# Kernel tuning notes

Hardware: AMD Instinct MI355X
Metric: run time of the kernel (lower is better)

Reference implementation:

```python
import jax, jax.numpy as jnp
import numpy as np

B = 2
D = 256          # conv_dim / d_model
NH = 8           # attention heads
NL = 3           # feature levels: res5, res4, res3 (forward iterates reversed)
NP = 4           # sampling points per head per level
NLAYERS = 6
FF = 1024
SHAPES = [(24, 24), (48, 48), (96, 96)]   # (H, W) per level in encoder order
LEN = sum(h * w for h, w in SHAPES)       # 12096
HD = D // NH


def group_norm(x, s, b, groups=32, eps=1e-5):
    Bb, C, H, W = x.shape
    xr = x.reshape(Bb, groups, C // groups, H, W)
    m = xr.mean((2, 3, 4), keepdims=True)
    v = xr.var((2, 3, 4), keepdims=True)
    xr = (xr - m) * jax.lax.rsqrt(v + eps)
    return xr.reshape(Bb, C, H, W) * s[:, None, None] + b[:, None, None]


def layer_norm(x, s, b, eps=1e-5):
    m = x.mean(-1, keepdims=True)
    v = x.var(-1, keepdims=True)
    return (x - m) * jax.lax.rsqrt(v + eps) * s + b


def pos_embed_sine(H, W):
    # PositionEmbeddingSine(num_pos_feats=D//2, normalize=True), mask=None
    num = D // 2
    eps = 1e-6
    scale = 2.0 * np.pi
    y = (jnp.arange(1, H + 1, dtype=jnp.float32) / (H + eps)) * scale
    x = (jnp.arange(1, W + 1, dtype=jnp.float32) / (W + eps)) * scale
    dim_t = 10000.0 ** (2.0 * (jnp.arange(num) // 2).astype(jnp.float32) / num)
    def enc(v):
        p = v[:, None] / dim_t
        return jnp.stack([jnp.sin(p[:, 0::2]), jnp.cos(p[:, 1::2])], -1).reshape(v.shape[0], num)
    pe_y, pe_x = enc(y), enc(x)
    pos = jnp.concatenate([
        jnp.broadcast_to(pe_y[:, None, :], (H, W, num)),
        jnp.broadcast_to(pe_x[None, :, :], (H, W, num))], -1)
    return pos.transpose(2, 0, 1)  # [D, H, W]


def ms_deform_sample(value, loc, attn):
    # value [B,LEN,NH,HD]; loc [B,LEN,NH,NL,NP,2] in [0,1] (x,y); attn [B,LEN,NH,NL,NP]
    # Equivalent to grid_sample(bilinear, padding=zeros, align_corners=False) per level.
    out = jnp.zeros((B * NH, LEN, HD), jnp.float32)
    start = 0
    for lvl, (H, W) in enumerate(SHAPES):
        v = value[:, start:start + H * W].transpose(0, 2, 1, 3).reshape(B * NH, H * W, HD)
        l = loc[:, :, :, lvl].transpose(0, 2, 1, 3, 4).reshape(B * NH, LEN * NP, 2)
        x = l[..., 0] * W - 0.5
        y = l[..., 1] * H - 0.5
        x0f = jnp.floor(x); y0f = jnp.floor(y)
        wx = x - x0f; wy = y - y0f
        x0 = x0f.astype(jnp.int32); y0 = y0f.astype(jnp.int32)
        def gather(yi, xi):
            valid = (xi >= 0) & (xi < W) & (yi >= 0) & (yi < H)
            idx = jnp.clip(yi, 0, H - 1) * W + jnp.clip(xi, 0, W - 1)
            g = jnp.take_along_axis(v, idx[..., None], axis=1)
            return g * valid[..., None]
        s = (gather(y0, x0) * ((1 - wx) * (1 - wy))[..., None]
             + gather(y0, x0 + 1) * (wx * (1 - wy))[..., None]
             + gather(y0 + 1, x0) * ((1 - wx) * wy)[..., None]
             + gather(y0 + 1, x0 + 1) * (wx * wy)[..., None])
        w = attn[:, :, :, lvl].transpose(0, 2, 1, 3).reshape(B * NH, LEN * NP)
        out = out + (s * w[..., None]).reshape(B * NH, LEN, NP, HD).sum(2)
        start += H * W
    return out.reshape(B, NH, LEN, HD).transpose(0, 2, 1, 3).reshape(B, LEN, D)


def upsample_bilinear(x, Ho, Wo):
    # F.interpolate(mode='bilinear', align_corners=False)
    Bb, C, H, W = x.shape
    ys = jnp.maximum((jnp.arange(Ho, dtype=jnp.float32) + 0.5) * (H / Ho) - 0.5, 0.0)
    xs = jnp.maximum((jnp.arange(Wo, dtype=jnp.float32) + 0.5) * (W / Wo) - 0.5, 0.0)
    y0 = jnp.floor(ys).astype(jnp.int32); wy = ys - y0
    x0 = jnp.floor(xs).astype(jnp.int32); wx = xs - x0
    y1 = jnp.minimum(y0 + 1, H - 1); x1 = jnp.minimum(x0 + 1, W - 1)
    r = x[:, :, y0, :] * (1 - wy)[None, None, :, None] + x[:, :, y1, :] * wy[None, None, :, None]
    return r[:, :, :, x0] * (1 - wx)[None, None, None, :] + r[:, :, :, x1] * wx[None, None, None, :]


def conv1x1(x, w):
    return jnp.einsum('bchw,oc->bohw', x, w)


def _forward(res2, res3, res4, res5,
             pw5, pb5, gs5, gb5, pw4, pb4, gs4, gb4, pw3, pb3, gs3, gb3,
             level_embed, off_w, off_b, aw_w, aw_b, val_w, val_b, out_w, out_b,
             ln1_s, ln1_b, ffn1_w, ffn1_b, ffn2_w, ffn2_b, ln2_s, ln2_b,
             lat_w, lat_gs, lat_gb, fpn_w, fpn_gs, fpn_gb):
    feats = [res5, res4, res3]  # transformer_in_features reversed (coarse -> fine)
    projs = [(pw5, pb5, gs5, gb5), (pw4, pb4, gs4, gb4), (pw3, pb3, gs3, gb3)]
    src_list, pos_list = [], []
    for f, (pw, pb, gs, gb) in zip(feats, projs):
        s = group_norm(conv1x1(f, pw) + pb[:, None, None], gs, gb)
        src_list.append(s.reshape(B, D, -1).transpose(0, 2, 1))
        pos_list.append(pos_embed_sine(f.shape[2], f.shape[3]))
    src = jnp.concatenate(src_list, axis=1)  # [B, LEN, D]
    pos = jnp.concatenate([p.reshape(D, -1).T + level_embed[i]
                           for i, p in enumerate(pos_list)], axis=0)[None]  # [1, LEN, D]
    # reference points (x, y), valid_ratios == 1 (no padding masks)
    refs = []
    for H, W in SHAPES:
        gy, gx = jnp.meshgrid((jnp.arange(H, dtype=jnp.float32) + 0.5) / H,
                              (jnp.arange(W, dtype=jnp.float32) + 0.5) / W, indexing='ij')
        refs.append(jnp.stack([gx.ravel(), gy.ravel()], -1))
    ref_pts = jnp.broadcast_to(jnp.concatenate(refs, 0)[None, :, None, :], (B, LEN, NL, 2))
    norm_wh = jnp.array([[W, H] for H, W in SHAPES], jnp.float32)  # offset normalizer (x=W, y=H)
    for l in range(NLAYERS):
        q = src + pos
        value = (src @ val_w[l] + val_b[l]).reshape(B, LEN, NH, HD)
        off = (q @ off_w[l] + off_b[l]).reshape(B, LEN, NH, NL, NP, 2)
        aw = jax.nn.softmax((q @ aw_w[l] + aw_b[l]).reshape(B, LEN, NH, NL * NP), -1)
        aw = aw.reshape(B, LEN, NH, NL, NP)
        loc = ref_pts[:, :, None, :, None, :] + off / norm_wh[None, None, None, :, None, :]
        attn = ms_deform_sample(value, loc, aw) @ out_w[l] + out_b[l]
        src = layer_norm(src + attn, ln1_s[l], ln1_b[l])
        h = jax.nn.relu(src @ ffn1_w[l] + ffn1_b[l]) @ ffn2_w[l] + ffn2_b[l]
        src = layer_norm(src + h, ln2_s[l], ln2_b[l])
    outs, start = [], 0
    for H, W in SHAPES:
        outs.append(src[:, start:start + H * W].transpose(0, 2, 1).reshape(B, D, H, W))
        start += H * W
    # FPN: single lateral/output level (res2)
    lat = group_norm(conv1x1(res2, lat_w), lat_gs, lat_gb)
    y = lat + upsample_bilinear(outs[-1], lat.shape[2], lat.shape[3])
    y = jax.lax.conv_general_dilated(y, fpn_w, (1, 1), 'SAME',
                                     dimension_numbers=('NCHW', 'OIHW', 'NCHW'))
    y = jax.nn.relu(group_norm(y, fpn_gs, fpn_gb))
    # returns (out[-1], out[0], multi_scale_features...) = (fpn, y_res5, y_res5, y_res4, y_res3)
    return y, outs[0], outs[1], outs[2]


def setup_inputs():
    ks = jax.random.split(jax.random.key(0), 40)
    def rn(i, shape, s=0.02):
        return jax.random.normal(ks[i], shape, jnp.float32) * s
    inp = {}
    inp['res2'] = jax.random.normal(ks[0], (B, 256, 192, 192), jnp.float32)
    inp['res3'] = jax.random.normal(ks[1], (B, 512, 96, 96), jnp.float32)
    inp['res4'] = jax.random.normal(ks[2], (B, 1024, 48, 48), jnp.float32)
    inp['res5'] = jax.random.normal(ks[3], (B, 2048, 24, 24), jnp.float32)
    for name, cin, i in [('5', 2048, 4), ('4', 1024, 5), ('3', 512, 6)]:
        inp['pw' + name] = rn(i, (D, cin))
        inp['pb' + name] = jnp.zeros((D,), jnp.float32)
        inp['gs' + name] = jnp.ones((D,), jnp.float32)
        inp['gb' + name] = jnp.zeros((D,), jnp.float32)
    inp['level_embed'] = rn(7, (NL, D), 1.0)
    inp['off_w'] = rn(8, (NLAYERS, D, NH * NL * NP * 2))
    inp['off_b'] = rn(9, (NLAYERS, NH * NL * NP * 2), 0.5)
    inp['aw_w'] = rn(10, (NLAYERS, D, NH * NL * NP))
    inp['aw_b'] = jnp.zeros((NLAYERS, NH * NL * NP), jnp.float32)
    inp['val_w'] = rn(11, (NLAYERS, D, D))
    inp['val_b'] = jnp.zeros((NLAYERS, D), jnp.float32)
    inp['out_w'] = rn(12, (NLAYERS, D, D))
    inp['out_b'] = jnp.zeros((NLAYERS, D), jnp.float32)
    inp['ln1_s'] = jnp.ones((NLAYERS, D), jnp.float32)
    inp['ln1_b'] = jnp.zeros((NLAYERS, D), jnp.float32)
    inp['ffn1_w'] = rn(13, (NLAYERS, D, FF))
    inp['ffn1_b'] = jnp.zeros((NLAYERS, FF), jnp.float32)
    inp['ffn2_w'] = rn(14, (NLAYERS, FF, D))
    inp['ffn2_b'] = jnp.zeros((NLAYERS, D), jnp.float32)
    inp['ln2_s'] = jnp.ones((NLAYERS, D), jnp.float32)
    inp['ln2_b'] = jnp.zeros((NLAYERS, D), jnp.float32)
    inp['lat_w'] = rn(15, (D, 256))
    inp['lat_gs'] = jnp.ones((D,), jnp.float32)
    inp['lat_gb'] = jnp.zeros((D,), jnp.float32)
    inp['fpn_w'] = rn(16, (D, D, 3, 3))
    inp['fpn_gs'] = jnp.ones((D,), jnp.float32)
    inp['fpn_gb'] = jnp.zeros((D,), jnp.float32)
    return inp


def reference(res2, res3, res4, res5,
              pw5, pb5, gs5, gb5, pw4, pb4, gs4, gb4, pw3, pb3, gs3, gb3,
              level_embed, off_w, off_b, aw_w, aw_b, val_w, val_b, out_w, out_b,
              ln1_s, ln1_b, ffn1_w, ffn1_b, ffn2_w, ffn2_b, ln2_s, ln2_b,
              lat_w, lat_gs, lat_gb, fpn_w, fpn_gs, fpn_gb):
    return _forward(res2, res3, res4, res5,
                    pw5, pb5, gs5, gb5, pw4, pb4, gs4, gb4, pw3, pb3, gs3, gb3,
                    level_embed, off_w, off_b, aw_w, aw_b, val_w, val_b, out_w, out_b,
                    ln1_s, ln1_b, ffn1_w, ffn1_b, ffn2_w, ffn2_b, ln2_s, ln2_b,
                    lat_w, lat_gs, lat_gb, fpn_w, fpn_gs, fpn_gb)
```

## Files before the change

### kernel.cpp

```cpp
#include <hip/hip_runtime.h>
#include <math.h>

#define NLEN 12096
#define BB 2

typedef __bf16 bhalf;
typedef bhalf bh8 __attribute__((ext_vector_type(8)));
typedef bhalf bh4 __attribute__((ext_vector_type(4)));
typedef float f32x4 __attribute__((ext_vector_type(4)));

__device__ __forceinline__ int swz(int row) { return (row >> 1) & 3; }

__device__ __forceinline__ int xcd_swz(int id, int nwg) {
  int q = nwg >> 3, r = nwg & 7;
  int xcd = id & 7, pos = id >> 3;
  int base = (xcd < r) ? xcd * (q + 1) : r * (q + 1) + (xcd - r) * q;
  return base + pos;
}

#define GLOAD_LDS16(g, l) \
  __builtin_amdgcn_global_load_lds( \
      (const __attribute__((address_space(1))) unsigned int*)(g), \
      (__attribute__((address_space(3))) unsigned int*)(l), 16, 0, 0)

__global__ __launch_bounds__(256) void bgemm_kernel(
    const bhalf* __restrict__ A, const bhalf* __restrict__ Bt,
    const float* __restrict__ bias, void* __restrict__ Cout,
    int M, int N, int K, long long sA, long long sB, long long sC,
    int outBf16, int relu)
{
  const int gx = gridDim.x, gy = gridDim.y;
  const int nwg = gx * gy * gridDim.z;
  int flat = (blockIdx.z * gy + blockIdx.y) * gx + blockIdx.x;
  int logical = xcd_swz(flat, nwg);
  const int bz = logical / (gx * gy);
  int rem = logical - bz * gx * gy;
  const int by = rem / gx;
  const int bx = rem - by * gx;

  A += bz * sA; Bt += bz * sB;
  const int m0 = by * 128, n0 = bx * 128;
  __shared__ __align__(16) bhalf As[128 * 32];
  __shared__ __align__(16) bhalf Bs[128 * 32];
  const int t = threadIdx.x;
  const int lane = t & 63;
  const int w = t >> 6;
  const int wbase = t & 192;
  const int wm = (w >> 1) * 64, wn = (w & 1) * 64;
  const int fr = lane & 15, fg = lane >> 4;
  f32x4 acc[4][4] = {};
  for (int k0 = 0; k0 < K; k0 += 32) {
#pragma unroll
    for (int j = 0; j < 2; ++j) {
      int id = t + j * 256;
      int row = id >> 2, up = id & 3;
      int kcg = ((up ^ swz(row)) * 8);
      int m = m0 + row; m = (m < M) ? m : (M - 1);
      GLOAD_LDS16(A + (long long)m * K + k0 + kcg, As + (wbase + j * 256) * 8);
      int n = n0 + row; n = (n < N) ? n : (N - 1);
      GLOAD_LDS16(Bt + (long long)n * K + k0 + kcg, Bs + (wbase + j * 256) * 8);
    }
    __syncthreads();
    bh8 af[4], bf[4];
#pragma unroll
    for (int mi = 0; mi < 4; ++mi) {
      int r = wm + mi * 16 + fr;
      af[mi] = *(const bh8*)(As + r * 32 + ((fg ^ swz(r)) * 8));
    }
#pragma unroll
    for (int ni = 0; ni < 4; ++ni) {
      int r = wn + ni * 16 + fr;
      bf[ni] = *(const bh8*)(Bs + r * 32 + ((fg ^ swz(r)) * 8));
    }
#pragma unroll
    for (int mi = 0; mi < 4; ++mi)
#pragma unroll
      for (int ni = 0; ni < 4; ++ni)
        acc[mi][ni] = __builtin_amdgcn_mfma_f32_16x16x32_bf16(af[mi], bf[ni], acc[mi][ni], 0, 0, 0);
    __syncthreads();
  }
  float* Cf = (float*)Cout + bz * sC;
  bhalf* Cb = (bhalf*)Cout + bz * sC;
#pragma unroll
  for (int mi = 0; mi < 4; ++mi) {
#pragma unroll
    for (int r = 0; r < 4; ++r) {
      int m = m0 + wm + mi * 16 + fg * 4 + r;
      if (m >= M) continue;
#pragma unroll
      for (int ni = 0; ni < 4; ++ni) {
        int n = n0 + wn + ni * 16 + fr;
        if (n >= N) continue;
        float v = acc[mi][ni][r];
        if (bias) v += bias[n];
        if (relu) v = fmaxf(v, 0.f);
        if (outBf16) Cb[(long long)m * N + n] = (bhalf)v;
        else         Cf[(long long)m * N + n] = v;
      }
    }
  }
}

__global__ __launch_bounds__(256) void bgemm_ln_kernel(
    const bhalf* __restrict__ A, const bhalf* __restrict__ Bt,
    const float* __restrict__ bias,
    float* __restrict__ src, bhalf* __restrict__ srcb,
    bhalf* __restrict__ qbOut, const float* __restrict__ pos,
    const float* __restrict__ ls, const float* __restrict__ lb,
    int M, int K)
{
  const int nwg = gridDim.x;
  const int bid = xcd_swz(blockIdx.x, nwg);
  const int m0 = bid * 64;
  __shared__ __align__(16) bhalf Ls[320 * 32];
  bhalf* AsL = Ls;
  bhalf* BsL = Ls + 64 * 32;
  __shared__ float shS[64][2], shQ[64][2];
  const int t = threadIdx.x;
  const int lane = t & 63;
  const int w = t >> 6;
  const int wbase = t & 192;
  const int wm = (w >> 1) * 32, wn = (w & 1) * 128;
  const int fr = lane & 15, fg = lane >> 4;
  f32x4 acc[2][8] = {};
  for (int k0 = 0; k0 < K; k0 += 32) {
#pragma unroll
    for (int j = 0; j < 5; ++j) {
      int id = t + j * 256;
      int row = id >> 2, up = id & 3;
      int kcg = ((up ^ swz(row)) * 8);
      const bhalf* gsrc = (row < 64)
          ? (A + (long long)(m0 + row) * K + k0 + kcg)
          : (Bt + (long long)(row - 64) * K + k0 + kcg);
      GLOAD_LDS16(gsrc, Ls + (wbase + j * 256) * 8);
    }
    __syncthreads();
    bh8 af[2], bf[8];
#pragma unroll
    for (int mi = 0; mi < 2; ++mi) {
      int r = wm + mi * 16 + fr;
      af[mi] = *(const bh8*)(AsL + r * 32 + ((fg ^ swz(r)) * 8));
    }
#pragma unroll
    for (int ni = 0; ni < 8; ++ni) {
      int r = wn + ni * 16 + fr;
      bf[ni] = *(const bh8*)(BsL + r * 32 + ((fg ^ swz(r)) * 8));
    }
#pragma unroll
    for (int mi = 0; mi < 2; ++mi)
#pragma unroll
      for (int ni = 0; ni < 8; ++ni)
        acc[mi][ni] = __builtin_amdgcn_mfma_f32_16x16x32_bf16(af[mi], bf[ni], acc[mi][ni], 0, 0, 0);
    __syncthreads();
  }
#pragma unroll
  for (int mi = 0; mi < 2; ++mi) {
#pragma unroll
    for (int r = 0; r < 4; ++r) {
      int rt = wm + mi * 16 + fg * 4 + r;
      long long gm = m0 + rt;
      float s = 0.f, q = 0.f;
#pragma unroll
      for (int ni = 0; ni < 8; ++ni) {
        int col = wn + ni * 16 + fr;
        float v = acc[mi][ni][r] + bias[col] + src[gm * 256 + col];
        acc[mi][ni][r] = v;
        s += v; q = fmaf(v, v, q);
      }
#pragma unroll
      for (int o = 1; o < 16; o <<= 1) { s += __shfl_xor(s, o); q += __shfl_xor(q, o); }
      if (fr == 0) { shS[rt][w & 1] = s; shQ[rt][w & 1] = q; }
    }
  }
  __syncthreads();
#pragma unroll
  for (int mi = 0; mi < 2; ++mi) {
#pragma unroll
    for (int r = 0; r < 4; ++r) {
      int rt = wm + mi * 16 + fg * 4 + r;
      long long gm = m0 + rt;
      float S = shS[rt][0] + shS[rt][1];
      float Q = shQ[rt][0] + shQ[rt][1];
      float mean = S * (1.f / 256.f);
      float var = Q * (1.f / 256.f) - mean * mean;
      float rstd = rsqrtf(var + 1e-5f);
      int prow = (int)(gm % NLEN);
#pragma unroll
      for (int ni = 0; ni < 8; ++ni) {
        int col = wn + ni * 16 + fr;
        float y = (acc[mi][ni][r] - mean) * rstd * ls[col] + lb[col];
        src[gm * 256 + col] = y;
        srcb[gm * 256 + col] = (bhalf)y;
        if (qbOut) qbOut[gm * 256 + col] = (bhalf)(y + pos[(long long)prow * 256 + col]);
      }
    }
  }
}

__global__ __launch_bounds__(256) void bgemm_conv_kernel(
    const bhalf* __restrict__ Ab, const bhalf* __restrict__ Bt,
    bhalf* __restrict__ Cout)
{
  const int gx = gridDim.x, gy = gridDim.y;
  const int nwg = gx * gy * gridDim.z;
  int flat = (blockIdx.z * gy + blockIdx.y) * gx + blockIdx.x;
  int logical = xcd_swz(flat, nwg);
  const int bz = logical / (gx * gy);
  int rem = logical - bz * gx * gy;
  const int by = rem / gx;
  const int bx = rem - by * gx;

  const bhalf* Apad = Ab + (long long)bz * 37636 * 256;
  const int m0 = by * 128, n0 = bx * 128;
  __shared__ __align__(16) bhalf As[128 * 32];
  __shared__ __align__(16) bhalf Bs[128 * 32];
  const int t = threadIdx.x;
  const int lane = t & 63;
  const int w = t >> 6;
  const int wbase = t & 192;
  const int wm = (w >> 1) * 64, wn = (w & 1) * 64;
  const int fr = lane & 15, fg = lane >> 4;
  int rowA[2], py[2], px[2], kcg[2];
#pragma unroll
  for (int j = 0; j < 2; ++j) {
    int id = t + j * 256;
    rowA[j] = id >> 2;
    kcg[j] = (((id & 3) ^ swz(rowA[j])) * 8);
    int m = m0 + rowA[j];
    py[j] = m / 192; px[j] = m % 192;
  }
  f32x4 acc[4][4] = {};
  for (int s = 0; s < 72; ++s) {
    const int cib = s / 9, tap = s % 9;
    const int ty = tap / 3, tx = tap % 3;
#pragma unroll
    for (int j = 0; j < 2; ++j) {
      GLOAD_LDS16(Apad + ((long long)(py[j] + ty) * 194 + px[j] + tx) * 256 + cib * 32 + kcg[j],
                  As + (wbase + j * 256) * 8);
      GLOAD_LDS16(Bt + (long long)(n0 + rowA[j]) * 2304 + s * 32 + kcg[j],
                  Bs + (wbase + j * 256) * 8);
    }
    __syncthreads();
    bh8 af[4], bf[4];
#pragma unroll
    for (int mi = 0; mi < 4; ++mi) {
      int r = wm + mi * 16 + fr;
      af[mi] = *(const bh8*)(As + r * 32 + ((fg ^ swz(r)) * 8));
    }
#pragma unroll
    for (int ni = 0; ni < 4; ++ni) {
      int r = wn + ni * 16 + fr;
      bf[ni] = *(const bh8*)(Bs + r * 32 + ((fg ^ swz(r)) * 8));
    }
#pragma unroll
    for (int mi = 0; mi < 4; ++mi)
#pragma unroll
      for (int ni = 0; ni < 4; ++ni)
        acc[mi][ni] = __builtin_amdgcn_mfma_f32_16x16x32_bf16(af[mi], bf[ni], acc[mi][ni], 0, 0, 0);
    __syncthreads();
  }
  bhalf* Cb = Cout + (long long)bz * 36864 * 256;
#pragma unroll
  for (int mi = 0; mi < 4; ++mi)
#pragma unroll
    for (int r = 0; r < 4; ++r) {
      int m = m0 + wm + mi * 16 + fg * 4 + r;
#pragma unroll
      for (int ni = 0; ni < 4; ++ni) {
        int n = n0 + wn + ni * 16 + fr;
        Cb[(long long)m * 256 + n] = (bhalf)acc[mi][ni][r];
      }
    }
}

__global__ void twcvt_kernel(const float* __restrict__ Wsrc, bhalf* __restrict__ out,
                             int Kd, int Nd, long long zdst)
{
  __shared__ float tile[32][33];
  long long zi = (long long)blockIdx.z * Kd * Nd;
  long long zo = (long long)blockIdx.z * zdst;
  int n0 = blockIdx.x * 32, k0 = blockIdx.y * 32;
#pragma unroll
  for (int j = 0; j < 4; ++j) {
    int kk = threadIdx.y + 8 * j;
    tile[kk][threadIdx.x] = Wsrc[zi + (long long)(k0 + kk) * Nd + n0 + threadIdx.x];
  }
  __syncthreads();
#pragma unroll
  for (int j = 0; j < 4; ++j) {
    int nn = threadIdx.y + 8 * j;
    out[zo + (long long)(n0 + nn) * Kd + k0 + threadIdx.x] = (bhalf)tile[threadIdx.x][nn];
  }
}

__global__ void tfeat_kernel(const float* __restrict__ Fsrc, bhalf* __restrict__ out,
                             int Ci, int HW)
{
  __shared__ float tile[32][33];
  long long zo = (long long)blockIdx.z * Ci * HW;
  int hw0 = blockIdx.x * 32, c0 = blockIdx.y * 32;
#pragma unroll
  for (int j = 0; j < 4; ++j) {
    int cc = threadIdx.y + 8 * j;
    tile[cc][threadIdx.x] = Fsrc[zo + (long long)(c0 + cc) * HW + hw0 + threadIdx.x];
  }
  __syncthreads();
#pragma unroll
  for (int j = 0; j < 4; ++j) {
    int hh = threadIdx.y + 8 * j;
    out[zo + (long long)(hw0 + hh) * Ci + c0 + threadIdx.x] = (bhalf)tile[threadIdx.x][hh];
  }
}

__global__ void cvt_kernel(const float* __restrict__ in, bhalf* __restrict__ out, int n)
{
  int i = blockIdx.x * 256 + threadIdx.x;
  if (i < n) out[i] = (bhalf)in[i];
}

__global__ void fpnw_kernel(const float* __restrict__ Wsrc, bhalf* __restrict__ out)
{
  int o = blockIdx.x * 256 + threadIdx.x;
  if (o >= 256 * 2304) return;
  int co = o / 2304, r = o % 2304;
  int cib = r / 288, rr = r % 288, tap = rr >> 5, cil = rr & 31;
  int ci = cib * 32 + cil;
  out[o] = (bhalf)Wsrc[(co * 256 + ci) * 9 + tap];
}

__global__ void biascat_kernel(const float* __restrict__ ob, const float* __restrict__ ab,
                               float* __restrict__ out)
{
  int l = blockIdx.x, t = threadIdx.x;
  if (t < 288) out[l * 288 + t] = (t < 192) ? ob[l * 192 + t] : ab[l * 96 + t - 192];
}

__global__ void border_zero_kernel(bhalf* __restrict__ latb)
{
  int idx = blockIdx.x * 256 + threadIdx.x;
  int total = BB * 4 * 194;
  if (idx >= total) return;
  int b = idx / (4 * 194);
  int r = idx - b * 4 * 194;
  int strip = r / 194, p = r % 194;
  int y, x;
  if (strip == 0)      { y = 0;   x = p; }
  else if (strip == 1) { y = 193; x = p; }
  else if (strip == 2) { y = p;   x = 0; }
  else                 { y = p;   x = 193; }
  uint4* dst = (uint4*)(latb + ((long long)b * 37636 + (long long)y * 194 + x) * 256);
#pragma unroll
  for (int j = 0; j < 32; ++j) dst[j] = make_uint4(0u, 0u, 0u, 0u);
}

__global__ void pos_kernel(float* __restrict__ pos, const float* __restrict__ level_embed)
{
  int i = blockIdx.x, c = threadIdx.x;
  int lvl, Wq, loc;
  if (i < 576)       { lvl = 0; Wq = 24; loc = i; }
  else if (i < 2880) { lvl = 1; Wq = 48; loc = i - 576; }
  else               { lvl = 2; Wq = 96; loc = i - 2880; }
  int h = loc / Wq, wcol = loc % Wq;
  int cc = c & 127;
  float coord = (c < 128) ? (float)(h + 1) : (float)(wcol + 1);
  float denom = (float)Wq + 1e-6f;
  float v = coord / denom * 6.28318530717958647692f;
  float tp = powf(10000.0f, (float)(cc & ~1) * (1.0f / 128.0f));
  float ang = v / tp;
  float val = (cc & 1) ? cosf(ang) : sinf(ang);
  pos[(long long)i * 256 + c] = val + level_embed[lvl * 256 + c];
}

__global__ __launch_bounds__(256) void gn_part_kernel(const void* __restrict__ X,
    float* __restrict__ part, int HW, int isBf16, int nch)
{
  const int b = blockIdx.y, ch = blockIdx.x;
  const int rows = (HW + nch - 1) / nch;
  const int r0 = ch * rows;
  const int r1 = min(r0 + rows, HW);
  const int cg = threadIdx.x & 31;
  const int ro = threadIdx.x >> 5;
  float s = 0.f, s2 = 0.f;
  if (isBf16) {
    const bhalf* p = (const bhalf*)X + (long long)b * HW * 256 + cg * 8;
    for (int r = r0 + ro; r < r1; r += 8) {
      bh8 v = *(const bh8*)(p + (long long)r * 256);
#pragma unroll
// ... 31 lines not shown
    long long o = ((long long)bg * nch + i) * 2;
    s += part[o]; s2 += part[o + 1];
  }
#pragma unroll
  for (int o = 32; o > 0; o >>= 1) { s += __shfl_down(s, o); s2 += __shfl_down(s2, o); }
  if (threadIdx.x == 0) {
    float inv = 1.f / (float)(HW * 8);
    float mean = s * inv;
    float var = s2 * inv - mean * mean;
    stats[bg * 2] = mean;
    stats[bg * 2 + 1] = rsqrtf(var + 1e-5f);
  }
}

__global__ void gn_apply_rm_kernel(const float* __restrict__ T, const float* __restrict__ stats,
    const float* __restrict__ gs, const float* __restrict__ gb,
    float* __restrict__ src, bhalf* __restrict__ srcb, bhalf* __restrict__ qb,
    const float* __restrict__ pos, int HW, int startRow)
{
  long long idx = (long long)blockIdx.x * 256 + threadIdx.x;
  int c = threadIdx.x & 255;
  long long row = idx >> 8;
  int b = (int)(row / HW);
  long long hw = row - (long long)b * HW;
  int g = c >> 3;
  float v = T[idx];
  v = (v - stats[(b * 32 + g) * 2]) * stats[(b * 32 + g) * 2 + 1] * gs[c] + gb[c];
  long long pr = (startRow + hw) * 256 + c;
  long long o = (long long)b * NLEN * 256 + pr;
  src[o] = v;
  srcb[o] = (bhalf)v;
  qb[o] = (bhalf)(v + pos[pr]);
}

__global__ __launch_bounds__(256) void deform_kernel(const bhalf* __restrict__ value,
    const bhalf* __restrict__ offaw, bhalf* __restrict__ out)
{
  const int t = threadIdx.x;
  const int q = t >> 5;
  const int sub = t & 31;
  const int bi = blockIdx.x * 8 + q;
  const int i = bi % NLEN;
  const int bbase = bi - i;
  const int c0 = sub * 8;
  const int head = sub >> 2;
  int loc, Wq;
  if (i < 576)       { Wq = 24; loc = i; }
  else if (i < 2880) { Wq = 48; loc = i - 576; }
  else               { Wq = 96; loc = i - 2880; }
  const float rx = ((loc % Wq) + 0.5f) / (float)Wq;
  const float ry = ((loc / Wq) + 0.5f) / (float)Wq;
  const bhalf* offp = offaw + (long long)bi * 288 + head * 24;
  const bhalf* awp  = offaw + (long long)bi * 288 + 192 + head * 12;
  float aw[12]; float mx = -1e30f;
#pragma unroll
  for (int j = 0; j < 12; ++j) { aw[j] = (float)awp[j]; mx = fmaxf(mx, aw[j]); }
  float ssum = 0.f;
#pragma unroll
  for (int j = 0; j < 12; ++j) { aw[j] = __expf(aw[j] - mx); ssum += aw[j]; }
  const float sinv = 1.f / ssum;
  float acc[8] = {};
  const int starts[3] = {0, 576, 2880};
  const int Ls[3] = {24, 48, 96};
#pragma unroll
  for (int l = 0; l < 3; ++l) {
    const int Wl = Ls[l];
    const float fW = (float)Wl;
    const bhalf* vb = value + (long long)(bbase + starts[l]) * 256 + c0;
#pragma unroll
    for (int p = 0; p < 4; ++p) {
      const float ox = (float)offp[l * 8 + p * 2], oy = (float)offp[l * 8 + p * 2 + 1];
      const float a = aw[l * 4 + p] * sinv;
      const float x = (rx + ox / fW) * fW - 0.5f;
      const float y = (ry + oy / fW) * fW - 0.5f;
      const float x0f = floorf(x), y0f = floorf(y);
      const float wx = x - x0f, wy = y - y0f;
      const int x0 = (int)x0f, y0 = (int)y0f;
      const int x1 = x0 + 1, y1 = y0 + 1;
      const bool xv0 = (x0 >= 0) & (x0 < Wl);
      const bool xv1 = (x1 >= 0) & (x1 < Wl);
      const bool yv0 = (y0 >= 0) & (y0 < Wl);
      const bool yv1 = (y1 >= 0) & (y1 < Wl);
      const int cx0 = min(max(x0, 0), Wl - 1), cx1 = min(max(x1, 0), Wl - 1);
      const int cy0 = min(max(y0, 0), Wl - 1), cy1 = min(max(y1, 0), Wl - 1);
      const float w00 = (xv0 && yv0) ? (1.f - wx) * (1.f - wy) * a : 0.f;
      const float w01 = (xv1 && yv0) ? wx * (1.f - wy) * a : 0.f;
      const float w10 = (xv0 && yv1) ? (1.f - wx) * wy * a : 0.f;
      const float w11 = (xv1 && yv1) ? wx * wy * a : 0.f;
      const bh8 g00 = *(const bh8*)(vb + (cy0 * Wl + cx0) * 256);
      const bh8 g01 = *(const bh8*)(vb + (cy0 * Wl + cx1) * 256);
      const bh8 g10 = *(const bh8*)(vb + (cy1 * Wl + cx0) * 256);
      const bh8 g11 = *(const bh8*)(vb + (cy1 * Wl + cx1) * 256);
#pragma unroll
      for (int e = 0; e < 8; ++e)
        acc[e] = fmaf(w00, (float)g00[e], fmaf(w01, (float)g01[e],
                 fmaf(w10, (float)g10[e], fmaf(w11, (float)g11[e], acc[e]))));
    }
  }
  bh8 o;
#pragma unroll
  for (int e = 0; e < 8; ++e) o[e] = (bhalf)acc[e];
  *(bh8*)(out + (long long)bi * 256 + c0) = o;
}

__global__ void transpose_out_kernel(const float* __restrict__ src, float* __restrict__ out,
    int HW, int startRow)
{
  __shared__ float tile[32][33];
  int b = blockIdx.z;
  int w0 = blockIdx.x * 32, c0 = blockIdx.y * 32;
#pragma unroll
  for (int j = 0; j < 4; ++j) {
    int wl = threadIdx.y + 8 * j;
    tile[wl][threadIdx.x] = src[((long long)b * NLEN + startRow + w0 + wl) * 256 + c0 + threadIdx.x];
  }
  __syncthreads();
#pragma unroll
  for (int j = 0; j < 4; ++j) {
    int cl = threadIdx.y + 8 * j;
    out[((long long)b * 256 + c0 + cl) * HW + w0 + threadIdx.x] = tile[threadIdx.x][cl];
  }
}

__global__ void lat_finish_rm_kernel(const bhalf* __restrict__ lat, const float* __restrict__ stats,
    const float* __restrict__ gs, const float* __restrict__ gb,
    const float* __restrict__ src, bhalf* __restrict__ latb)
{
  long long idx = (long long)blockIdx.x * 256 + threadIdx.x;
  int c = threadIdx.x & 255;
  long long row = idx >> 8;
  int b = (int)(row / 36864);
  int p = (int)(row - (long long)b * 36864);
  int y = p / 192, x = p % 192;
  int g = c >> 3;
  float v = (float)lat[idx];
  v = (v - stats[(b * 32 + g) * 2]) * stats[(b * 32 + g) * 2 + 1] * gs[c] + gb[c];
  float ys = fmaxf(y * 0.5f - 0.25f, 0.f);
  float xs = fmaxf(x * 0.5f - 0.25f, 0.f);
  int y0 = (int)ys; float wy = ys - (float)y0; int y1 = min(y0 + 1, 95);
  int x0 = (int)xs; float wx = xs - (float)x0; int x1 = min(x0 + 1, 95);
  const float* sp = src + ((long long)b * NLEN + 2880) * 256 + c;
  float r0 = sp[(long long)(y0 * 96 + x0) * 256] * (1.f - wx) + sp[(long long)(y0 * 96 + x1) * 256] * wx;
  float r1 = sp[(long long)(y1 * 96 + x0) * 256] * (1.f - wx) + sp[(long long)(y1 * 96 + x1) * 256] * wx;
  latb[((long long)b * 37636 + (long long)(y + 1) * 194 + (x + 1)) * 256 + c]
      = (bhalf)(v + r0 * (1.f - wy) + r1 * wy);
}

__global__ void gn_relu_tr_kernel(const bhalf* __restrict__ convC, const float* __restrict__ stats,
    const float* __restrict__ gs, const float* __restrict__ gb, float* __restrict__ Y)
{
  __shared__ float tile[32][33];
  int b = blockIdx.z;
  int hw0 = blockIdx.x * 32, c0 = blockIdx.y * 32;
#pragma unroll
  for (int j = 0; j < 4; ++j) {
    int hwl = threadIdx.y + 8 * j;
    int c = c0 + threadIdx.x;
    int g = c >> 3;
    float v = (float)convC[((long long)b * 36864 + hw0 + hwl) * 256 + c];
    v = (v - stats[(b * 32 + g) * 2]) * stats[(b * 32 + g) * 2 + 1] * gs[c] + gb[c];
    tile[hwl][threadIdx.x] = fmaxf(v, 0.f);
  }
  __syncthreads();
// ... 29 lines not shown
  const float* ln1_b = (const float*)d_in[26];
  const float* ffn1_w = (const float*)d_in[27];
  const float* ffn1_b = (const float*)d_in[28];
  const float* ffn2_w = (const float*)d_in[29];
  const float* ffn2_b = (const float*)d_in[30];
  const float* ln2_s = (const float*)d_in[31];
  const float* ln2_b = (const float*)d_in[32];
  const float* lat_w = (const float*)d_in[33];
  const float* lat_gs = (const float*)d_in[34];
  const float* lat_gb = (const float*)d_in[35];
  const float* fpn_w = (const float*)d_in[36];
  const float* fpn_gs = (const float*)d_in[37];
  const float* fpn_gb = (const float*)d_in[38];

  char* W = (char*)d_ws;
  float* src   = (float*)(W + 0);
  float* pos   = (float*)(W + 24772608LL);
  float* tmp   = (float*)(W + 37158912LL);
  bhalf* srcb  = (bhalf*)(W + 61931520LL);
  bhalf* wreg  = (bhalf*)(W + 74317824LL);
  float* stats = (float*)(W + 86212608LL);
  float* part  = (float*)(W + 86213120LL);
  float* offaw_b = (float*)(W + 86278656LL);
  char*  U     = W + 86286848LL;

  bhalf* valT   = wreg + 0;
  bhalf* offawT = wreg + 393216;
  bhalf* outT   = wreg + 835584;
  bhalf* f1T    = wreg + 1228800;
  bhalf* f2T    = wreg + 2801664;
  bhalf* pwb5   = wreg + 4374528;
  bhalf* pwb4   = wreg + 4898816;
  bhalf* pwb3   = wreg + 5160960;
  bhalf* latwb  = wreg + 5292032;
  bhalf* fpnT   = wreg + 5357568;

  bhalf* qb      = (bhalf*)(U + 0);
  bhalf* valueb  = (bhalf*)(U + 12386304LL);
  bhalf* sampb   = (bhalf*)(U + 24772608LL);
  bhalf* offbuf  = (bhalf*)(U + 37158912LL);
  bhalf* hbuf    = (bhalf*)(U + 65028096LL);
  bhalf* featT   = (bhalf*)(U + 24772608LL);
  bhalf* res2T   = (bhalf*)(U + 0);
  bhalf* latbf   = (bhalf*)(U + 37748736LL);
  bhalf* latb    = (bhalf*)(U + 75497472LL);

  float* Yout = (float*)d_out;
  float* out0 = Yout + 18874368LL;
  float* out1 = Yout + 19169280LL;
  float* out2 = Yout + 20348928LL;

  const int M = BB * NLEN;

  twcvt_kernel<<<dim3(8, 8, 6), dim3(32, 8), 0, stream>>>(val_w, valT, 256, 256, 65536LL);
  twcvt_kernel<<<dim3(6, 8, 6), dim3(32, 8), 0, stream>>>(off_w, offawT, 256, 192, 73728LL);
  twcvt_kernel<<<dim3(3, 8, 6), dim3(32, 8), 0, stream>>>(aw_w, offawT + 192 * 256, 256, 96, 73728LL);
  twcvt_kernel<<<dim3(8, 8, 6), dim3(32, 8), 0, stream>>>(out_w, outT, 256, 256, 65536LL);
  twcvt_kernel<<<dim3(32, 8, 6), dim3(32, 8), 0, stream>>>(ffn1_w, f1T, 256, 1024, 262144LL);
  twcvt_kernel<<<dim3(8, 32, 6), dim3(32, 8), 0, stream>>>(ffn2_w, f2T, 1024, 256, 262144LL);
  biascat_kernel<<<dim3(6), dim3(288), 0, stream>>>(off_b, aw_b, offaw_b);
  cvt_kernel<<<dim3(2048), dim3(256), 0, stream>>>(pw[0], pwb5, 524288);
  cvt_kernel<<<dim3(1024), dim3(256), 0, stream>>>(pw[1], pwb4, 262144);
  cvt_kernel<<<dim3(512),  dim3(256), 0, stream>>>(pw[2], pwb3, 131072);
  cvt_kernel<<<dim3(256),  dim3(256), 0, stream>>>(lat_w, latwb, 65536);
  fpnw_kernel<<<dim3(2304), dim3(256), 0, stream>>>(fpn_w, fpnT);

  pos_kernel<<<dim3(NLEN), dim3(256), 0, stream>>>(pos, level_embed);

  const float* feats[3] = {res5, res4, res3};
  const bhalf* pwbs[3] = {pwb5, pwb4, pwb3};
  const int cins[3] = {2048, 1024, 512};
  const int HWs[3] = {576, 2304, 9216};
  const int startsHost[3] = {0, 576, 2880};
  const int nchs[3] = {16, 64, 128};
  for (int lvl = 0; lvl < 3; ++lvl) {
    int HW = HWs[lvl], cin = cins[lvl], nch = nchs[lvl];
    tfeat_kernel<<<dim3(HW / 32, cin / 32, BB), dim3(32, 8), 0, stream>>>(feats[lvl], featT, cin, HW);
    bgemm_kernel<<<dim3(2, (HW + 127) / 128, BB), dim3(256), 0, stream>>>(
        featT, pwbs[lvl], pb[lvl], tmp, HW, 256, cin,
        (long long)HW * cin, 0LL, (long long)HW * 256, 0, 0);
    gn_part_kernel<<<dim3(nch, BB), dim3(256), 0, stream>>>(tmp, part, HW, 0, nch);
    gn_fin_kernel<<<dim3(64), dim3(64), 0, stream>>>(part, stats, nch, HW);
    gn_apply_rm_kernel<<<dim3(BB * HW), dim3(256), 0, stream>>>(
        tmp, stats, gss[lvl], gbb[lvl], src, srcb, qb, pos, HW, startsHost[lvl]);
  }

  for (int l = 0; l < 6; ++l) {
    bgemm_kernel<<<dim3(2, M / 128, 1), dim3(256), 0, stream>>>(
        srcb, valT + (long long)l * 65536, val_b + l * 256, valueb,
        M, 256, 256, 0LL, 0LL, 0LL, 1, 0);
    bgemm_kernel<<<dim3(3, M / 128, 1), dim3(256), 0, stream>>>(
        qb, offawT + (long long)l * 73728, offaw_b + l * 288, offbuf,
        M, 288, 256, 0LL, 0LL, 0LL, 1, 0);
    deform_kernel<<<dim3(M / 8), dim3(256), 0, stream>>>(valueb, offbuf, sampb);
    bgemm_ln_kernel<<<dim3(M / 64), dim3(256), 0, stream>>>(
        sampb, outT + (long long)l * 65536, out_b + l * 256,
        src, srcb, nullptr, pos, ln1_s + l * 256, ln1_b + l * 256, M, 256);
    bgemm_kernel<<<dim3(8, M / 128, 1), dim3(256), 0, stream>>>(
        srcb, f1T + (long long)l * 262144, ffn1_b + l * 1024, hbuf,
        M, 1024, 256, 0LL, 0LL, 0LL, 1, 1);
    bgemm_ln_kernel<<<dim3(M / 64), dim3(256), 0, stream>>>(
        hbuf, f2T + (long long)l * 262144, ffn2_b + l * 256,
        src, srcb, qb, pos, ln2_s + l * 256, ln2_b + l * 256, M, 1024);
  }

  float* outsPtr[3] = {out0, out1, out2};
  for (int lvl = 0; lvl < 3; ++lvl) {
    transpose_out_kernel<<<dim3(HWs[lvl] / 32, 8, BB), dim3(32, 8), 0, stream>>>(
        src, outsPtr[lvl], HWs[lvl], startsHost[lvl]);
  }

  tfeat_kernel<<<dim3(1152, 8, BB), dim3(32, 8), 0, stream>>>(res2, res2T, 256, 36864);
  bgemm_kernel<<<dim3(2, 288, BB), dim3(256), 0, stream>>>(
      res2T, latwb, nullptr, latbf, 36864, 256, 256,
      36864LL * 256, 0LL, 36864LL * 256, 1, 0);
  gn_part_kernel<<<dim3(128, BB), dim3(256), 0, stream>>>(latbf, part, 36864, 1, 128);
  gn_fin_kernel<<<dim3(64), dim3(64), 0, stream>>>(part, stats, 128, 36864);
  border_zero_kernel<<<dim3((BB * 4 * 194 + 255) / 256), dim3(256), 0, stream>>>(latb);
  lat_finish_rm_kernel<<<dim3(73728), dim3(256), 0, stream>>>(latbf, stats, lat_gs, lat_gb, src, latb);
  bgemm_conv_kernel<<<dim3(2, 288, BB), dim3(256), 0, stream>>>(latb, fpnT, latbf);
  gn_part_kernel<<<dim3(128, BB), dim3(256), 0, stream>>>(latbf, part, 36864, 1, 128);
  gn_fin_kernel<<<dim3(64), dim3(64), 0, stream>>>(part, stats, 128, 36864);
  gn_relu_tr_kernel<<<dim3(1152, 8, BB), dim3(32, 8), 0, stream>>>(latbf, stats, fpn_gs, fpn_gb, Yout);
}
```

Baseline: 1.771 ms.

## Narrow GEMM tiles, halve LN-GEMM row tile, merge prep and transpose launches

Measured after the change: 1.582 ms. 10.7% less time.

```diff
diff --git a/kernel.cpp b/kernel.cpp
--- a/kernel.cpp
+++ b/kernel.cpp
@@ -23,12 +23,18 @@
       (const __attribute__((address_space(1))) unsigned int*)(g), \
       (__attribute__((address_space(3))) unsigned int*)(l), 16, 0, 0)
 
-__global__ __launch_bounds__(256) void bgemm_kernel(
+template<int BNF>
+__global__ __launch_bounds__(256) void bgemm_t_kernel(
     const bhalf* __restrict__ A, const bhalf* __restrict__ Bt,
     const float* __restrict__ bias, void* __restrict__ Cout,
     int M, int N, int K, long long sA, long long sB, long long sC,
     int outBf16, int relu)
 {
+  constexpr int BN = BNF * 16;
+  constexpr int ROWS = 128 + BN;
+  constexpr int UNITS = ROWS * 4;
+  constexpr int ITERS = (UNITS + 255) / 256;
+  constexpr int NFR = BNF / 2;
   const int gx = gridDim.x, gy = gridDim.y;
   const int nwg = gx * gy * gridDim.z;
   int flat = (blockIdx.z * gy + blockIdx.y) * gx + blockIdx.x;
@@ -39,43 +45,49 @@
   const int bx = rem - by * gx;
 
   A += bz * sA; Bt += bz * sB;
-  const int m0 = by * 128, n0 = bx * 128;
-  __shared__ __align__(16) bhalf As[128 * 32];
-  __shared__ __align__(16) bhalf Bs[128 * 32];
+  const int m0 = by * 128, n0 = bx * BN;
+  __shared__ __align__(16) bhalf Ls[ROWS * 32];
   const int t = threadIdx.x;
   const int lane = t & 63;
   const int w = t >> 6;
   const int wbase = t & 192;
-  const int wm = (w >> 1) * 64, wn = (w & 1) * 64;
+  const int wm = (w >> 1) * 64, wn = (w & 1) * (BN / 2);
   const int fr = lane & 15, fg = lane >> 4;
-  f32x4 acc[4][4] = {};
+  f32x4 acc[4][NFR] = {};
   for (int k0 = 0; k0 < K; k0 += 32) {
 #pragma unroll
-    for (int j = 0; j < 2; ++j) {
-      int id = t + j * 256;
-      int row = id >> 2, up = id & 3;
-      int kcg = ((up ^ swz(row)) * 8);
-      int m = m0 + row; m = (m < M) ? m : (M - 1);
-      GLOAD_LDS16(A + (long long)m * K + k0 + kcg, As + (wbase + j * 256) * 8);
-      int n = n0 + row; n = (n < N) ? n : (N - 1);
-      GLOAD_LDS16(Bt + (long long)n * K + k0 + kcg, Bs + (wbase + j * 256) * 8);
+    for (int j = 0; j < ITERS; ++j) {
+      int u = t + j * 256;
+      if (UNITS % 256 == 0 || u < UNITS) {
+        int row = u >> 2, up = u & 3;
+        int kcg = ((up ^ swz(row)) * 8);
+        const bhalf* gsrc;
+        if (row < 128) {
+          int m = m0 + row; m = (m < M) ? m : (M - 1);
+          gsrc = A + (long long)m * K + k0 + kcg;
+        } else {
+          int n = n0 + row - 128; n = (n < N) ? n : (N - 1);
+          gsrc = Bt + (long long)n * K + k0 + kcg;
+        }
+        GLOAD_LDS16(gsrc, Ls + (long long)(wbase + j * 256) * 8);
+      }
     }
     __syncthreads();
-    bh8 af[4], bf[4];
+    bh8 af[4], bf[NFR];
 #pragma unroll
     for (int mi = 0; mi < 4; ++mi) {
       int r = wm + mi * 16 + fr;
-      af[mi] = *(const bh8*)(As + r * 32 + ((fg ^ swz(r)) * 8));
-    }
-#pragma unroll
-    for (int ni = 0; ni < 4; ++ni) {
-      int r = wn + ni * 16 + fr;
-      bf[ni] = *(const bh8*)(Bs + r * 32 + ((fg ^ swz(r)) * 8));
+      af[mi] = *(const bh8*)(Ls + r * 32 + ((fg ^ swz(r)) * 8));
+    }
+#pragma unroll
+    for (int ni = 0; ni < NFR; ++ni) {
+      int r = 128 + wn + ni * 16 + fr;
+      bf[ni] = *(const bh8*)(Ls + r * 32 + ((fg ^ swz(r)) * 8));
     }
 #pragma unroll
     for (int mi = 0; mi < 4; ++mi)
 #pragma unroll
-      for (int ni = 0; ni < 4; ++ni)
+      for (int ni = 0; ni < NFR; ++ni)
         acc[mi][ni] = __builtin_amdgcn_mfma_f32_16x16x32_bf16(af[mi], bf[ni], acc[mi][ni], 0, 0, 0);
     __syncthreads();
   }
@@ -88,7 +100,7 @@
       int m = m0 + wm + mi * 16 + fg * 4 + r;
       if (m >= M) continue;
 #pragma unroll
-      for (int ni = 0; ni < 4; ++ni) {
+      for (int ni = 0; ni < NFR; ++ni) {
         int n = n0 + wn + ni * 16 + fr;
         if (n >= N) continue;
         float v = acc[mi][ni][r];
@@ -111,88 +123,79 @@
 {
   const int nwg = gridDim.x;
   const int bid = xcd_swz(blockIdx.x, nwg);
-  const int m0 = bid * 64;
-  __shared__ __align__(16) bhalf Ls[320 * 32];
-  bhalf* AsL = Ls;
-  bhalf* BsL = Ls + 64 * 32;
-  __shared__ float shS[64][2], shQ[64][2];
+  const int m0 = bid * 32;
+  __shared__ __align__(16) bhalf Ls[288 * 32];
+  __shared__ float shS[32][2], shQ[32][2];
   const int t = threadIdx.x;
   const int lane = t & 63;
   const int w = t >> 6;
   const int wbase = t & 192;
-  const int wm = (w >> 1) * 32, wn = (w & 1) * 128;
+  const int wm = (w >> 1) * 16, wn = (w & 1) * 128;
   const int fr = lane & 15, fg = lane >> 4;
-  f32x4 acc[2][8] = {};
+  f32x4 acc[8] = {};
   for (int k0 = 0; k0 < K; k0 += 32) {
 #pragma unroll
     for (int j = 0; j < 5; ++j) {
-      int id = t + j * 256;
-      int row = id >> 2, up = id & 3;
-      int kcg = ((up ^ swz(row)) * 8);
-      const bhalf* gsrc = (row < 64)
-          ? (A + (long long)(m0 + row) * K + k0 + kcg)
-          : (Bt + (long long)(row - 64) * K + k0 + kcg);
-      GLOAD_LDS16(gsrc, Ls + (wbase + j * 256) * 8);
+      int u = t + j * 256;
+      if (u < 1152) {
+        int row = u >> 2, up = u & 3;
+        int kcg = ((up ^ swz(row)) * 8);
+        const bhalf* gsrc = (row < 32)
+            ? (A + (long long)(m0 + row) * K + k0 + kcg)
+            : (Bt + (long long)(row - 32) * K + k0 + kcg);
+        GLOAD_LDS16(gsrc, Ls + (long long)(wbase + j * 256) * 8);
+      }
     }
     __syncthreads();
-    bh8 af[2], bf[8];
-#pragma unroll
-    for (int mi = 0; mi < 2; ++mi) {
-      int r = wm + mi * 16 + fr;
-      af[mi] = *(const bh8*)(AsL + r * 32 + ((fg ^ swz(r)) * 8));
+    bh8 af, bf[8];
+    {
+      int r = wm + fr;
+      af = *(const bh8*)(Ls + r * 32 + ((fg ^ swz(r)) * 8));
     }
 #pragma unroll
     for (int ni = 0; ni < 8; ++ni) {
-      int r = wn + ni * 16 + fr;
-      bf[ni] = *(const bh8*)(BsL + r * 32 + ((fg ^ swz(r)) * 8));
-    }
-#pragma unroll
-    for (int mi = 0; mi < 2; ++mi)
-#pragma unroll
-      for (int ni = 0; ni < 8; ++ni)
-        acc[mi][ni] = __builtin_amdgcn_mfma_f32_16x16x32_bf16(af[mi], bf[ni], acc[mi][ni], 0, 0, 0);
+      int r = 32 + wn + ni * 16 + fr;
+      bf[ni] = *(const bh8*)(Ls + r * 32 + ((fg ^ swz(r)) * 8));
+    }
+#pragma unroll
+    for (int ni = 0; ni < 8; ++ni)
+      acc[ni] = __builtin_amdgcn_mfma_f32_16x16x32_bf16(af, bf[ni], acc[ni], 0, 0, 0);
     __syncthreads();
   }
 #pragma unroll
-  for (int mi = 0; mi < 2; ++mi) {
-#pragma unroll
-    for (int r = 0; r < 4; ++r) {
-      int rt = wm + mi * 16 + fg * 4 + r;
-      long long gm = m0 + rt;
-      float s = 0.f, q = 0.f;
-#pragma unroll
-      for (int ni = 0; ni < 8; ++ni) {
-        int col = wn + ni * 16 + fr;
-        float v = acc[mi][ni][r] + bias[col] + src[gm * 256 + col];
-        acc[mi][ni][r] = v;
-        s += v; q = fmaf(v, v, q);
-      }
-#pragma unroll
-      for (int o = 1; o < 16; o <<= 1) { s += __shfl_xor(s, o); q += __shfl_xor(q, o); }
-      if (fr == 0) { shS[rt][w & 1] = s; shQ[rt][w & 1] = q; }
-    }
+  for (int r = 0; r < 4; ++r) {
+    int rt = wm + fg * 4 + r;
+    long long gm = m0 + rt;
+    float s = 0.f, q = 0.f;
+#pragma unroll
+    for (int ni = 0; ni < 8; ++ni) {
+      int col = wn + ni * 16 + fr;
+      float v = acc[ni][r] + bias[col] + src[gm * 256 + col];
+      acc[ni][r] = v;
+      s += v; q = fmaf(v, v, q);
+    }
+#pragma unroll
+    for (int o = 1; o < 16; o <<= 1) { s += __shfl_xor(s, o); q += __shfl_xor(q, o); }
+    if (fr == 0) { shS[rt][w & 1] = s; shQ[rt][w & 1] = q; }
   }
   __syncthreads();
 #pragma unroll
-  for (int mi = 0; mi < 2; ++mi) {
-#pragma unroll
-    for (int r = 0; r < 4; ++r) {
-      int rt = wm + mi * 16 + fg * 4 + r;
-      long long gm = m0 + rt;
-      float S = shS[rt][0] + shS[rt][1];
-      float Q = shQ[rt][0] + shQ[rt][1];
-      float mean = S * (1.f / 256.f);
-      float var = Q * (1.f / 256.f) - mean * mean;
-      float rstd = rsqrtf(var + 1e-5f);
-      int prow = (int)(gm % NLEN);
-#pragma unroll
-      for (int ni = 0; ni < 8; ++ni) {
-        int col = wn + ni * 16 + fr;
-        float y = (acc[mi][ni][r] - mean) * rstd * ls[col] + lb[col];
-        src[gm * 256 + col] = y;
-        srcb[gm * 256 + col] = (bhalf)y;
-        if (qbOut) qbOut[gm * 256 + col] = (bhalf)(y + pos[(long long)prow * 256 + col]);
-      }
+  for (int r = 0; r < 4; ++r) {
+    int rt = wm + fg * 4 + r;
+    long long gm = m0 + rt;
+    float S = shS[rt][0] + shS[rt][1];
+    float Q = shQ[rt][0] + shQ[rt][1];
+    float mean = S * (1.f / 256.f);
+    float var = Q * (1.f / 256.f) - mean * mean;
+    float rstd = rsqrtf(var + 1e-5f);
+    int prow = (int)(gm % NLEN);
+#pragma unroll
+    for (int ni = 0; ni < 8; ++ni) {
+      int col = wn + ni * 16 + fr;
+      float y = (acc[ni][r] - mean) * rstd * ls[col] + lb[col];
+      src[gm * 256 + col] = y;
+      srcb[gm * 256 + col] = (bhalf)y;
+      if (qbOut) qbOut[gm * 256 + col] = (bhalf)(y + pos[(long long)prow * 256 + col]);
     }
   }
 }
@@ -273,13 +276,36 @@
     }
 }
 
-__global__ void twcvt_kernel(const float* __restrict__ Wsrc, bhalf* __restrict__ out,
-                             int Kd, int Nd, long long zdst)
-{
+__global__ void wprep_t_kernel(
+    const float* __restrict__ s0, const float* __restrict__ s1,
+    const float* __restrict__ s2, const float* __restrict__ s3,
+    const float* __restrict__ s4, const float* __restrict__ s5,
+    bhalf* __restrict__ d0, bhalf* __restrict__ d1, bhalf* __restrict__ d2,
+    bhalf* __restrict__ d3, bhalf* __restrict__ d4, bhalf* __restrict__ d5)
+{
+  const int KdA[6]  = {256, 256, 256, 256, 256, 1024};
+  const int NdA[6]  = {256, 192, 96, 256, 1024, 256};
+  const long long zdA[6] = {65536, 73728, 73728, 65536, 262144, 262144};
+  const int cum[6]  = {384, 672, 816, 1200, 2736, 4272};
+  int blk = blockIdx.x;
+  int seg = 0;
+#pragma unroll
+  for (int i = 0; i < 6; ++i) if (blk >= cum[i]) seg = i + 1;
+  int base = (seg == 0) ? 0 : cum[seg - 1];
+  int idx = blk - base;
+  const float* Wsrc = (seg == 0) ? s0 : (seg == 1) ? s1 : (seg == 2) ? s2
+                    : (seg == 3) ? s3 : (seg == 4) ? s4 : s5;
+  bhalf* out = (seg == 0) ? d0 : (seg == 1) ? d1 : (seg == 2) ? d2
+             : (seg == 3) ? d3 : (seg == 4) ? d4 : d5;
+  int Kd = KdA[seg], Nd = NdA[seg];
+  int nx = Nd / 32, ny = Kd / 32;
+  int z = idx / (nx * ny);
+  int r = idx - z * nx * ny;
+  int ky = r / nx, nxi = r - ky * nx;
   __shared__ float tile[32][33];
-  long long zi = (long long)blockIdx.z * Kd * Nd;
-  long long zo = (long long)blockIdx.z * zdst;
-  int n0 = blockIdx.x * 32, k0 = blockIdx.y * 32;
+  long long zi = (long long)z * Kd * Nd;
+  long long zo = (long long)z * zdA[seg];
+  int n0 = nxi * 32, k0 = ky * 32;
 #pragma unroll
   for (int j = 0; j < 4; ++j) {
     int kk = threadIdx.y + 8 * j;
@@ -293,6 +319,39 @@
   }
 }
 
+__global__ void wprep_m_kernel(
+    const float* __restrict__ fpn_w, bhalf* __restrict__ fpnT,
+    const float* __restrict__ pw5, bhalf* __restrict__ pwb5,
+    const float* __restrict__ pw4, bhalf* __restrict__ pwb4,
+    const float* __restrict__ pw3, bhalf* __restrict__ pwb3,
+    const float* __restrict__ lat_w, bhalf* __restrict__ latwb,
+    const float* __restrict__ ob, const float* __restrict__ ab,
+    float* __restrict__ offaw_b)
+{
+  int blk = blockIdx.x, t = threadIdx.x;
+  if (blk < 2304) {
+    int o = blk * 256 + t;
+    int co = o / 2304, r = o % 2304;
+    int cib = r / 288, rr = r % 288, tap = rr >> 5, cil = rr & 31;
+    int ci = cib * 32 + cil;
+    fpnT[o] = (bhalf)fpn_w[(co * 256 + ci) * 9 + tap];
+  } else if (blk < 4352) {
+    int i = (blk - 2304) * 256 + t; pwb5[i] = (bhalf)pw5[i];
+  } else if (blk < 5376) {
+    int i = (blk - 4352) * 256 + t; pwb4[i] = (bhalf)pw4[i];
+  } else if (blk < 5888) {
+    int i = (blk - 5376) * 256 + t; pwb3[i] = (bhalf)pw3[i];
+  } else if (blk < 6144) {
+    int i = (blk - 5888) * 256 + t; latwb[i] = (bhalf)lat_w[i];
+  } else {
+    int i = (blk - 6144) * 256 + t;
+    if (i < 6 * 288) {
+      int l = i / 288, c = i % 288;
+      offaw_b[i] = (c < 192) ? ob[l * 192 + c] : ab[l * 96 + c - 192];
+    }
+  }
+}
+
 __global__ void tfeat_kernel(const float* __restrict__ Fsrc, bhalf* __restrict__ out,
                              int Ci, int HW)
 {
@@ -310,29 +369,6 @@
     int hh = threadIdx.y + 8 * j;
     out[zo + (long long)(hw0 + hh) * Ci + c0 + threadIdx.x] = (bhalf)tile[threadIdx.x][hh];
   }
-}
-
-__global__ void cvt_kernel(const float* __restrict__ in, bhalf* __restrict__ out, int n)
-{
-  int i = blockIdx.x * 256 + threadIdx.x;
-  if (i < n) out[i] = (bhalf)in[i];
-}
-
-__global__ void fpnw_kernel(const float* __restrict__ Wsrc, bhalf* __restrict__ out)
-{
-  int o = blockIdx.x * 256 + threadIdx.x;
-  if (o >= 256 * 2304) return;
-  int co = o / 2304, r = o % 2304;
-  int cib = r / 288, rr = r % 288, tap = rr >> 5, cil = rr & 31;
-  int ci = cib * 32 + cil;
-  out[o] = (bhalf)Wsrc[(co * 256 + ci) * 9 + tap];
-}
-
-__global__ void biascat_kernel(const float* __restrict__ ob, const float* __restrict__ ab,
-                               float* __restrict__ out)
-{
-  int l = blockIdx.x, t = threadIdx.x;
-  if (t < 288) out[l * 288 + t] = (t < 192) ? ob[l * 192 + t] : ab[l * 96 + t - 192];
 }
 
 __global__ void border_zero_kernel(bhalf* __restrict__ latb)
@@ -470,12 +506,10 @@
   const float ry = ((loc / Wq) + 0.5f) / (float)Wq;
   const bhalf* offp = offaw + (long long)bi * 288 + head * 24;
   const bhalf* awp  = offaw + (long long)bi * 288 + 192 + head * 12;
-  float aw[12]; float mx = -1e30f;
-#pragma unroll
-  for (int j = 0; j < 12; ++j) { aw[j] = (float)awp[j]; mx = fmaxf(mx, aw[j]); }
+  float aw[12];
   float ssum = 0.f;
 #pragma unroll
-  for (int j = 0; j < 12; ++j) { aw[j] = __expf(aw[j] - mx); ssum += aw[j]; }
+  for (int j = 0; j < 12; ++j) { aw[j] = __expf((float)awp[j]); ssum += aw[j]; }
   const float sinv = 1.f / ssum;
   float acc[8] = {};
   const int starts[3] = {0, 576, 2880};
@@ -521,12 +555,20 @@
   *(bh8*)(out + (long long)bi * 256 + c0) = o;
 }
 
-__global__ void transpose_out_kernel(const float* __restrict__ src, float* __restrict__ out,
-    int HW, int startRow)
-{
+__global__ void transpose_out_kernel(const float* __restrict__ src,
+    float* __restrict__ out0, float* __restrict__ out1, float* __restrict__ out2)
+{
+  int blk = blockIdx.x;
+  int lvl, HW, startRow;
+  float* out;
+  if (blk < 288)       { lvl = 0; HW = 576;  startRow = 0;    out = out0; }
+  else if (blk < 1440) { lvl = 1; HW = 2304; startRow = 576;  out = out1; blk -= 288; }
+  else                 { lvl = 2; HW = 9216; startRow = 2880; out = out2; blk -= 1440; }
+  int nx = HW / 32;
+  int bx = blk % nx; int r = blk / nx;
+  int cy = r % 8; int b = r / 8;
   __shared__ float tile[32][33];
-  int b = blockIdx.z;
-  int w0 = blockIdx.x * 32, c0 = blockIdx.y * 32;
+  int w0 = bx * 32, c0 = cy * 32;
 #pragma unroll
   for (int j = 0; j < 4; ++j) {
     int wl = threadIdx.y + 8 * j;
@@ -662,18 +704,12 @@
 
   const int M = BB * NLEN;
 
-  twcvt_kernel<<<dim3(8, 8, 6), dim3(32, 8), 0, stream>>>(val_w, valT, 256, 256, 65536LL);
-  twcvt_kernel<<<dim3(6, 8, 6), dim3(32, 8), 0, stream>>>(off_w, offawT, 256, 192, 73728LL);
-  twcvt_kernel<<<dim3(3, 8, 6), dim3(32, 8), 0, stream>>>(aw_w, offawT + 192 * 256, 256, 96, 73728LL);
-  twcvt_kernel<<<dim3(8, 8, 6), dim3(32, 8), 0, stream>>>(out_w, outT, 256, 256, 65536LL);
-  twcvt_kernel<<<dim3(32, 8, 6), dim3(32, 8), 0, stream>>>(ffn1_w, f1T, 256, 1024, 262144LL);
-  twcvt_kernel<<<dim3(8, 32, 6), dim3(32, 8), 0, stream>>>(ffn2_w, f2T, 1024, 256, 262144LL);
-  biascat_kernel<<<dim3(6), dim3(288), 0, stream>>>(off_b, aw_b, offaw_b);
-  cvt_kernel<<<dim3(2048), dim3(256), 0, stream>>>(pw[0], pwb5, 524288);
-  cvt_kernel<<<dim3(1024), dim3(256), 0, stream>>>(pw[1], pwb4, 262144);
-  cvt_kernel<<<dim3(512),  dim3(256), 0, stream>>>(pw[2], pwb3, 131072);
-  cvt_kernel<<<dim3(256),  dim3(256), 0, stream>>>(lat_w, latwb, 65536);
-  fpnw_kernel<<<dim3(2304), dim3(256), 0, stream>>>(fpn_w, fpnT);
+  wprep_t_kernel<<<dim3(4272), dim3(32, 8), 0, stream>>>(
+      val_w, off_w, aw_w, out_w, ffn1_w, ffn2_w,
+      valT, offawT, offawT + 192 * 256, outT, f1T, f2T);
+  wprep_m_kernel<<<dim3(6151), dim3(256), 0, stream>>>(
+      fpn_w, fpnT, pw[0], pwb5, pw[1], pwb4, pw[2], pwb3,
+      lat_w, latwb, off_b, aw_b, offaw_b);
 
   pos_kernel<<<dim3(NLEN), dim3(256), 0, stream>>>(pos, level_embed);
 
@@ -686,7 +722,7 @@
   for (int lvl = 0; lvl < 3; ++lvl) {
     int HW = HWs[lvl], cin = cins[lvl], nch = nchs[lvl];
     tfeat_kernel<<<dim3(HW / 32, cin / 32, BB), dim3(32, 8), 0, stream>>>(feats[lvl], featT, cin, HW);
-    bgemm_kernel<<<dim3(2, (HW + 127) / 128, BB), dim3(256), 0, stream>>>(
+    bgemm_t_kernel<4><<<dim3(4, (HW + 127) / 128, BB), dim3(256), 0, stream>>>(
         featT, pwbs[lvl], pb[lvl], tmp, HW, 256, cin,
         (long long)HW * cin, 0LL, (long long)HW * 256, 0, 0);
     gn_part_kernel<<<dim3(nch, BB), dim3(256), 0, stream>>>(tmp, part, HW, 0, nch);
@@ -696,32 +732,28 @@
   }
 
   for (int l = 0; l < 6; ++l) {
-    bgemm_kernel<<<dim3(2, M / 128, 1), dim3(256), 0, stream>>>(
+    bgemm_t_kernel<4><<<dim3(4, M / 128, 1), dim3(256), 0, stream>>>(
         srcb, valT + (long long)l * 65536, val_b + l * 256, valueb,
         M, 256, 256, 0LL, 0LL, 0LL, 1, 0);
-    bgemm_kernel<<<dim3(3, M / 128, 1), dim3(256), 0, stream>>>(
+    bgemm_t_kernel<6><<<dim3(3, M / 128, 1), dim3(256), 0, stream>>>(
         qb, offawT + (long long)l * 73728, offaw_b + l * 288, offbuf,
         M, 288, 256, 0LL, 0LL, 0LL, 1, 0);
     deform_kernel<<<dim3(M / 8), dim3(256), 0, stream>>>(valueb, offbuf, sampb);
-    bgemm_ln_kernel<<<dim3(M / 64), dim3(256), 0, stream>>>(
+    bgemm_ln_kernel<<<dim3(M / 32), dim3(256), 0, stream>>>(
         sampb, outT + (long long)l * 65536, out_b + l * 256,
         src, srcb, nullptr, pos, ln1_s + l * 256, ln1_b + l * 256, M, 256);
-    bgemm_kernel<<<dim3(8, M / 128, 1), dim3(256), 0, stream>>>(
+    bgemm_t_kernel<8><<<dim3(8, M / 128, 1), dim3(256), 0, stream>>>(
         srcb, f1T + (long long)l * 262144, ffn1_b + l * 1024, hbuf,
         M, 1024, 256, 0LL, 0LL, 0LL, 1, 1);
-    bgemm_ln_kernel<<<dim3(M / 64), dim3(256), 0, stream>>>(
+    bgemm_ln_kernel<<<dim3(M / 32), dim3(256), 0, stream>>>(
         hbuf, f2T + (long long)l * 262144, ffn2_b + l * 256,
         src, srcb, qb, pos, ln2_s + l * 256, ln2_b + l * 256, M, 1024);
   }
 
-  float* outsPtr[3] = {out0, out1, out2};
-  for (int lvl = 0; lvl < 3; ++lvl) {
-    transpose_out_kernel<<<dim3(HWs[lvl] / 32, 8, BB), dim3(32, 8), 0, stream>>>(
-        src, outsPtr[lvl], HWs[lvl], startsHost[lvl]);
-  }
+  transpose_out_kernel<<<dim3(6048), dim3(32, 8), 0, stream>>>(src, out0, out1, out2);
 
   tfeat_kernel<<<dim3(1152, 8, BB), dim3(32, 8), 0, stream>>>(res2, res2T, 256, 36864);
-  bgemm_kernel<<<dim3(2, 288, BB), dim3(256), 0, stream>>>(
+  bgemm_t_kernel<4><<<dim3(4, 288, BB), dim3(256), 0, stream>>>(
       res2T, latwb, nullptr, latbf, 36864, 256, 256,
       36864LL * 256, 0LL, 36864LL * 256, 1, 0);
   gn_part_kernel<<<dim3(128, BB), dim3(256), 0, stream>>>(latbf, part, 36864, 1, 128);
```
